# Kernel tuning notes

Hardware: AMD Instinct MI355X
Metric: run time of the kernel (lower is better)

## Reference

```python
import jax, jax.numpy as jnp
import numpy as np

N_HEAD = 16

def setup_inputs() -> dict:
    key = jax.random.key(0)
    k1, k2, k3, k4, k5 = jax.random.split(key, 5)
    B, T, C = 4, 2048, 1024
    s = 0.02
    x = jax.random.normal(k1, (B, T, C), dtype=jnp.float32)
    W_attn = jax.random.normal(k2, (C, 3 * C), dtype=jnp.float32) * s
    b_attn = jnp.zeros((3 * C,), dtype=jnp.float32)
    W_proj = jax.random.normal(k3, (C, C), dtype=jnp.float32) * s
    b_proj = jnp.zeros((C,), dtype=jnp.float32)
    return {"x": x, "W_attn": W_attn, "b_attn": b_attn, "W_proj": W_proj, "b_proj": b_proj}

def reference(x, W_attn, b_attn, W_proj, b_proj):
    B, T, C = x.shape
    H = N_HEAD
    hd = C // H
    qkv = x @ W_attn + b_attn                       # [B,T,3C]
    q, k, v = jnp.split(qkv, 3, axis=-1)            # each [B,T,C]
    # [B,H,T,hd]
    q = q.reshape(B, T, H, hd).transpose(0, 2, 1, 3)
    k = k.reshape(B, T, H, hd).transpose(0, 2, 1, 3)
    v = v.reshape(B, T, H, hd).transpose(0, 2, 1, 3)
    att = jnp.einsum('bhqd,bhkd->bhqk', q, k) * (1.0 / jnp.sqrt(jnp.float32(hd)))
    causal = jnp.tril(jnp.ones((T, T), dtype=bool))
    att = jnp.where(causal[None, None], att, jnp.float32(-jnp.inf))
    att = jax.nn.softmax(att, axis=-1)
    y = jnp.einsum('bhqk,bhkd->bhqd', att, v)       # [B,H,T,hd]
    y = y.transpose(0, 2, 1, 3).reshape(B, T, C)
    return y @ W_proj + b_proj
```

## Files before the change

### kernel.cpp

```cpp
#include <hip/hip_runtime.h>
#include <hip/hip_bf16.h>

typedef __bf16 bf16x8 __attribute__((ext_vector_type(8)));
typedef float f32x4 __attribute__((ext_vector_type(4)));

static __device__ __forceinline__ unsigned short f32_to_bf16(float f) {
    union { float f; unsigned u; } v; v.f = f;
    unsigned u = v.u;
    u += 0x7FFFu + ((u >> 16) & 1u);
    return (unsigned short)(u >> 16);
}

static __device__ __forceinline__ void async_load16(const unsigned short* g,
                                                    unsigned short* l) {
    __builtin_amdgcn_global_load_lds(
        (__attribute__((address_space(1))) const unsigned int*)(const void*)g,
        (__attribute__((address_space(3))) unsigned int*)(void*)l,
        16, 0, 0);
}

__global__ void cast_f32_bf16(const float* __restrict__ src,
                              unsigned short* __restrict__ dst, int n4) {
    int i = blockIdx.x * blockDim.x + threadIdx.x;
    if (i < n4) {
        float4 f = ((const float4*)src)[i];
        ushort4 o;
        o.x = f32_to_bf16(f.x); o.y = f32_to_bf16(f.y);
        o.z = f32_to_bf16(f.z); o.w = f32_to_bf16(f.w);
        ((ushort4*)dst)[i] = o;
    }
}

__global__ void transpose_cast(const float* __restrict__ src,
                               unsigned short* __restrict__ dst, int R, int C) {
    __shared__ float tile[32][33];
    int c0 = blockIdx.x * 32, r0 = blockIdx.y * 32;
    int tx = threadIdx.x, ty = threadIdx.y;
    #pragma unroll
    for (int i = 0; i < 32; i += 8)
        tile[ty + i][tx] = src[(long)(r0 + ty + i) * C + c0 + tx];
    __syncthreads();
    #pragma unroll
    for (int i = 0; i < 32; i += 8)
        dst[(long)(c0 + ty + i) * R + r0 + tx] = f32_to_bf16(tile[tx][ty + i]);
}

template<bool OUT_BF16>
__global__ __launch_bounds__(256) void gemm_bt_bias(
    const unsigned short* __restrict__ A,
    const unsigned short* __restrict__ Bt,
    const float* __restrict__ bias,
    void* __restrict__ Cout,
    int M, int N, int K)
{
    __shared__ __align__(16) unsigned short As[128 * 32];
    __shared__ __align__(16) unsigned short Bs[128 * 32];

    const int tid  = threadIdx.x;
    const int m0   = blockIdx.x * 128;
    const int n0   = blockIdx.y * 128;
    const int w    = tid >> 6, lane = tid & 63;
    const int quad = lane >> 4, lr = lane & 15;
    const int wm   = (w >> 1) * 64, wn = (w & 1) * 64;

    f32x4 acc[4][4];
    #pragma unroll
    for (int i = 0; i < 4; i++)
        #pragma unroll
        for (int j = 0; j < 4; j++)
            acc[i][j] = (f32x4){0.f, 0.f, 0.f, 0.f};

    const int srow = lane >> 2;
    const int soff = (lane & 3) * 8;
    const unsigned short* gA0 = &A [(long)(m0 + w * 16 + srow) * K + soff];
    const unsigned short* gA1 = &A [(long)(m0 + 64 + w * 16 + srow) * K + soff];
    const unsigned short* gB0 = &Bt[(long)(n0 + w * 16 + srow) * K + soff];
    const unsigned short* gB1 = &Bt[(long)(n0 + 64 + w * 16 + srow) * K + soff];
    unsigned short* lA0 = &As[(w * 16) * 32];
    unsigned short* lA1 = &As[(64 + w * 16) * 32];
    unsigned short* lB0 = &Bs[(w * 16) * 32];
    unsigned short* lB1 = &Bs[(64 + w * 16) * 32];

    for (int k0 = 0; k0 < K; k0 += 32) {
        __syncthreads();
        async_load16(gA0 + k0, lA0);
        async_load16(gA1 + k0, lA1);
        async_load16(gB0 + k0, lB0);
        async_load16(gB1 + k0, lB1);
        __syncthreads();

        bf16x8 af[4], bfr[4];
        #pragma unroll
        for (int i = 0; i < 4; i++)
            af[i] = *(const bf16x8*)&As[(wm + i * 16 + lr) * 32 + quad * 8];
        #pragma unroll
        for (int j = 0; j < 4; j++)
            bfr[j] = *(const bf16x8*)&Bs[(wn + j * 16 + lr) * 32 + quad * 8];
        #pragma unroll
        for (int i = 0; i < 4; i++)
            #pragma unroll
            for (int j = 0; j < 4; j++)
                acc[i][j] = __builtin_amdgcn_mfma_f32_16x16x32_bf16(af[i], bfr[j], acc[i][j], 0, 0, 0);
    }

    #pragma unroll
    for (int i = 0; i < 4; i++) {
        #pragma unroll
        for (int j = 0; j < 4; j++) {
            int gcol = n0 + wn + j * 16 + lr;
            float bv = bias[gcol];
            #pragma unroll
            for (int r = 0; r < 4; r++) {
                int grow = m0 + wm + i * 16 + quad * 4 + r;
                float v = acc[i][j][r] + bv;
                if (OUT_BF16)
                    ((unsigned short*)Cout)[(long)grow * N + gcol] = f32_to_bf16(v);
                else
                    ((float*)Cout)[(long)grow * N + gcol] = v;
            }
        }
    }
}

__global__ __launch_bounds__(256) void transpose_v(
    const unsigned short* __restrict__ qkv,
    unsigned short* __restrict__ vT,
    int T, int C3, int C, int H)
{
    __shared__ __align__(16) unsigned short tile[64 * 72];
    const int tid = threadIdx.x;
    const int t0 = blockIdx.x * 64, h = blockIdx.y, b = blockIdx.z;
    const long ibase = ((long)b * T + t0) * C3 + 2 * C + h * 64;
    #pragma unroll
    for (int c = tid; c < 512; c += 256) {
        int r = c >> 3, off = (c & 7) * 8;
        *(uint4*)&tile[r * 72 + off] = *(const uint4*)&qkv[ibase + (long)r * C3 + off];
    }
    __syncthreads();
    const long obase = (long)((b * H + h) * 64) * T + t0;
    #pragma unroll
    for (int c = tid; c < 512; c += 256) {
        int d = c & 63, tc = c >> 6;
        unsigned short tmp[8];
        #pragma unroll
        for (int j = 0; j < 8; j++)
            tmp[j] = tile[(tc * 8 + j) * 72 + d];
        *(uint4*)&vT[obase + (long)d * T + tc * 8] = *(const uint4*)tmp;
    }
}

__global__ __launch_bounds__(256, 2) void attn_mfma(
    const unsigned short* __restrict__ qkv,
    const unsigned short* __restrict__ vT,
    unsigned short* __restrict__ yb,
    int T, int C3, int C, int H, int NT)
{
    constexpr int SQ = 72;
    __shared__ __align__(16) unsigned short Qs[128 * SQ];
    __shared__ __align__(16) unsigned short Ks[64 * SQ];
    __shared__ __align__(16) unsigned short Vs[64 * SQ];
    __shared__ __align__(16) unsigned short Ps[128 * SQ];

    const int tid = threadIdx.x;
    const int h   = blockIdx.y;
    const int b   = blockIdx.z;
    const long rowbase = (long)b * T;
    const long vtbase  = (long)((b * H + h) * 64) * T;

    const int w = tid >> 6, lane = tid & 63;
    const int quad = lane >> 4, lr = lane & 15;

    const int r0 = tid >> 3, off0 = (tid & 7) * 8;
    const int r1 = r0 + 32;

    const float scale2 = 0.1803368801111244f;

    for (int t = 0; t < 2; t++) {
        const int qt = (t == 0) ? blockIdx.x : (NT - 1 - blockIdx.x);
        const int q0 = qt * 128;
        const int nb = 2 * qt + 2;

        __syncthreads();

        #pragma unroll
        for (int i = 0; i < 4; i++)
            *(uint4*)&Qs[(r0 + i * 32) * SQ + off0] =
                *(const uint4*)&qkv[(rowbase + q0 + r0 + i * 32) * C3 + h * 64 + off0];

        uint4 pk0, pk1, pv0, pv1;
        {
            long g0 = (rowbase + r0) * (long)C3 + C + h * 64 + off0;
            long g1 = (rowbase + r1) * (long)C3 + C + h * 64 + off0;
            pk0 = *(const uint4*)&qkv[g0];
            pk1 = *(const uint4*)&qkv[g1];
            pv0 = *(const uint4*)&vT[vtbase + (long)r0 * T + off0];
            pv1 = *(const uint4*)&vT[vtbase + (long)r1 * T + off0];
        }

        f32x4 oA[2][4];
        float lp[8];
        #pragma unroll
        for (int st = 0; st < 2; st++)
            #pragma unroll
            for (int j = 0; j < 4; j++) oA[st][j] = (f32x4){0.f, 0.f, 0.f, 0.f};
        #pragma unroll
        for (int i = 0; i < 8; i++) lp[i] = 0.f;

        const int wrow0 = w * 32;
        const int wrowmax = q0 + wrow0 + 31;

        for (int kb = 0; kb < nb; kb++) {
            __syncthreads();
            *(uint4*)&Ks[r0 * SQ + off0] = pk0;
            *(uint4*)&Ks[r1 * SQ + off0] = pk1;
            *(uint4*)&Vs[r0 * SQ + off0] = pv0;
            *(uint4*)&Vs[r1 * SQ + off0] = pv1;
            __syncthreads();

            if (kb + 1 < nb) {
                long g0 = (rowbase + (kb + 1) * 64 + r0) * (long)C3 + C + h * 64 + off0;
                long g1 = (rowbase + (kb + 1) * 64 + r1) * (long)C3 + C + h * 64 + off0;
                pk0 = *(const uint4*)&qkv[g0];
                pk1 = *(const uint4*)&qkv[g1];
                pv0 = *(const uint4*)&vT[vtbase + (long)r0 * T + (kb + 1) * 64 + off0];
                pv1 = *(const uint4*)&vT[vtbase + (long)r1 * T + (kb + 1) * 64 + off0];
            }

            if (kb * 64 > wrowmax) continue;

            f32x4 sA[2][4];
            #pragma unroll
            for (int st = 0; st < 2; st++)
                #pragma unroll
                for (int j = 0; j < 4; j++) sA[st][j] = (f32x4){0.f, 0.f, 0.f, 0.f};
            #pragma unroll
            for (int ks = 0; ks < 2; ks++) {
                bf16x8 aq0 = *(const bf16x8*)&Qs[(wrow0 + lr) * SQ + ks * 32 + quad * 8];
                bf16x8 aq1 = *(const bf16x8*)&Qs[(wrow0 + 16 + lr) * SQ + ks * 32 + quad * 8];
                #pragma unroll
                for (int jt = 0; jt < 4; jt++) {
                    bf16x8 bk = *(const bf16x8*)&Ks[(jt * 16 + lr) * SQ + ks * 32 + quad * 8];
                    sA[0][jt] = __builtin_amdgcn_mfma_f32_16x16x32_bf16(aq0, bk, sA[0][jt], 0, 0, 0);
                    sA[1][jt] = __builtin_amdgcn_mfma_f32_16x16x32_bf16(aq1, bk, sA[1][jt], 0, 0, 0);
                }
            }

            const bool diag = (kb >= nb - 2);
            #pragma unroll
            for (int st = 0; st < 2; st++) {
                #pragma unroll
                for (int r = 0; r < 4; r++) {
                    int rowin = q0 + wrow0 + st * 16 + quad * 4 + r;
                    #pragma unroll
                    for (int jt = 0; jt < 4; jt++) {
                        float sv = sA[st][jt][r] * scale2;
                        if (diag && (kb * 64 + jt * 16 + lr) > rowin) sv = -1e30f;
                        float p = exp2f(fminf(sv, 80.f));
                        lp[st * 4 + r] += p;
                        Ps[(wrow0 + st * 16 + quad * 4 + r) * SQ + jt * 16 + lr] = f32_to_bf16(p);
                    }
                }
            }

            #pragma unroll
            for (int ks = 0; ks < 2; ks++) {
                bf16x8 ap0 = *(const bf16x8*)&Ps[(wrow0 + lr) * SQ + ks * 32 + quad * 8];
                bf16x8 ap1 = *(const bf16x8*)&Ps[(wrow0 + 16 + lr) * SQ + ks * 32 + quad * 8];
                #pragma unroll
                for (int jt = 0; jt < 4; jt++) {
                    bf16x8 bv = *(const bf16x8*)&Vs[(jt * 16 + lr) * SQ + ks * 32 + quad * 8];
                    oA[0][jt] = __builtin_amdgcn_mfma_f32_16x16x32_bf16(ap0, bv, oA[0][jt], 0, 0, 0);
                    oA[1][jt] = __builtin_amdgcn_mfma_f32_16x16x32_bf16(ap1, bv, oA[1][jt], 0, 0, 0);
                }
            }
        }

        #pragma unroll
        for (int st = 0; st < 2; st++) {
            #pragma unroll
            for (int r = 0; r < 4; r++) {
                float l = lp[st * 4 + r];
                l += __shfl_xor(l, 1);
                l += __shfl_xor(l, 2);
                l += __shfl_xor(l, 4);
                l += __shfl_xor(l, 8);
                float inv = 1.f / l;
                long grow = rowbase + q0 + wrow0 + st * 16 + quad * 4 + r;
                #pragma unroll
                for (int jt = 0; jt < 4; jt++)
                    yb[grow * C + h * 64 + jt * 16 + lr] = f32_to_bf16(oA[st][jt][r] * inv);
            }
        }
    }
}

extern "C" void kernel_launch(void* const* d_in, const int* in_sizes, int n_in,
                              void* d_out, int out_size, void* d_ws, size_t ws_size,
                              hipStream_t stream) {
    const float* x      = (const float*)d_in[0];
    const float* W_attn = (const float*)d_in[1];
    const float* b_attn = (const float*)d_in[2];
    const float* W_proj = (const float*)d_in[3];
    const float* b_proj = (const float*)d_in[4];
    float* out = (float*)d_out;

    const int B = 4, T = 2048, C = 1024, H = 16;
    const int M  = B * T;
    const int C3 = 3 * C;
    const int NT = T / 128;

    char* ws = (char*)d_ws;
    size_t off = 0;
    auto carve = [&](size_t bytes) {
        char* p = ws + off;
        off += (bytes + 255) & ~(size_t)255;
        return p;
    };
    unsigned short* xb   = (unsigned short*)carve((size_t)M * C * 2);
    unsigned short* wat  = (unsigned short*)carve((size_t)C3 * C * 2);
    unsigned short* wpt  = (unsigned short*)carve((size_t)C * C * 2);
    unsigned short* qkvb = (unsigned short*)carve((size_t)M * C3 * 2);
    unsigned short* ybuf = (unsigned short*)carve((size_t)M * C * 2);
    unsigned short* vTb  = xb;

    cast_f32_bf16<<<(M * C / 4 + 255) / 256, 256, 0, stream>>>(x, xb, M * C / 4);
    transpose_cast<<<dim3(C3 / 32, C / 32), dim3(32, 8), 0, stream>>>(W_attn, wat, C, C3);
    transpose_cast<<<dim3(C / 32, C / 32), dim3(32, 8), 0, stream>>>(W_proj, wpt, C, C);

    gemm_bt_bias<true><<<dim3(M / 128, C3 / 128), 256, 0, stream>>>(
        xb, wat, b_attn, qkvb, M, C3, C);

    transpose_v<<<dim3(T / 64, H, B), 256, 0, stream>>>(qkvb, vTb, T, C3, C, H);

    attn_mfma<<<dim3(NT / 2, H, B), 256, 0, stream>>>(qkvb, vTb, ybuf, T, C3, C, H, NT);

    gemm_bt_bias<false><<<dim3(M / 128, C / 128), 256, 0, stream>>>(
        ybuf, wpt, b_proj, out, M, C, C);
}
```

Baseline: 297.4 us.

## Fold softmax scale into QKV GEMM and keep Q fragments in registers

```diff
diff --git a/kernel.cpp b/kernel.cpp
--- a/kernel.cpp
+++ b/kernel.cpp
@@ -51,7 +51,7 @@
     const unsigned short* __restrict__ Bt,
     const float* __restrict__ bias,
     void* __restrict__ Cout,
-    int M, int N, int K)
+    int M, int N, int K, int scale_ncols, float scale)
 {
     __shared__ __align__(16) unsigned short As[128 * 32];
     __shared__ __align__(16) unsigned short Bs[128 * 32];
@@ -109,10 +109,11 @@
         for (int j = 0; j < 4; j++) {
             int gcol = n0 + wn + j * 16 + lr;
             float bv = bias[gcol];
+            float sc = (gcol < scale_ncols) ? scale : 1.0f;
             #pragma unroll
             for (int r = 0; r < 4; r++) {
                 int grow = m0 + wm + i * 16 + quad * 4 + r;
-                float v = acc[i][j][r] + bv;
+                float v = (acc[i][j][r] + bv) * sc;
                 if (OUT_BF16)
                     ((unsigned short*)Cout)[(long)grow * N + gcol] = f32_to_bf16(v);
                 else
@@ -149,14 +150,13 @@
     }
 }
 
-__global__ __launch_bounds__(256, 2) void attn_mfma(
+__global__ __launch_bounds__(256, 4) void attn_mfma(
     const unsigned short* __restrict__ qkv,
     const unsigned short* __restrict__ vT,
     unsigned short* __restrict__ yb,
     int T, int C3, int C, int H, int NT)
 {
     constexpr int SQ = 72;
-    __shared__ __align__(16) unsigned short Qs[128 * SQ];
     __shared__ __align__(16) unsigned short Ks[64 * SQ];
     __shared__ __align__(16) unsigned short Vs[64 * SQ];
     __shared__ __align__(16) unsigned short Ps[128 * SQ];
@@ -173,19 +173,21 @@
     const int r0 = tid >> 3, off0 = (tid & 7) * 8;
     const int r1 = r0 + 32;
 
-    const float scale2 = 0.1803368801111244f;
-
     for (int t = 0; t < 2; t++) {
         const int qt = (t == 0) ? blockIdx.x : (NT - 1 - blockIdx.x);
         const int q0 = qt * 128;
         const int nb = 2 * qt + 2;
 
-        __syncthreads();
-
-        #pragma unroll
-        for (int i = 0; i < 4; i++)
-            *(uint4*)&Qs[(r0 + i * 32) * SQ + off0] =
-                *(const uint4*)&qkv[(rowbase + q0 + r0 + i * 32) * C3 + h * 64 + off0];
+        const int wrow0 = w * 32;
+        const int wrowmax = q0 + wrow0 + 31;
+
+        bf16x8 aq[2][2];
+        #pragma unroll
+        for (int st = 0; st < 2; st++)
+            #pragma unroll
+            for (int ks = 0; ks < 2; ks++)
+                aq[st][ks] = *(const bf16x8*)&qkv[
+                    (rowbase + q0 + wrow0 + st * 16 + lr) * (long)C3 + h * 64 + ks * 32 + quad * 8];
 
         uint4 pk0, pk1, pv0, pv1;
         {
@@ -206,9 +208,6 @@
         #pragma unroll
         for (int i = 0; i < 8; i++) lp[i] = 0.f;
 
-        const int wrow0 = w * 32;
-        const int wrowmax = q0 + wrow0 + 31;
-
         for (int kb = 0; kb < nb; kb++) {
             __syncthreads();
             *(uint4*)&Ks[r0 * SQ + off0] = pk0;
@@ -235,13 +234,11 @@
                 for (int j = 0; j < 4; j++) sA[st][j] = (f32x4){0.f, 0.f, 0.f, 0.f};
             #pragma unroll
             for (int ks = 0; ks < 2; ks++) {
-                bf16x8 aq0 = *(const bf16x8*)&Qs[(wrow0 + lr) * SQ + ks * 32 + quad * 8];
-                bf16x8 aq1 = *(const bf16x8*)&Qs[(wrow0 + 16 + lr) * SQ + ks * 32 + quad * 8];
                 #pragma unroll
                 for (int jt = 0; jt < 4; jt++) {
                     bf16x8 bk = *(const bf16x8*)&Ks[(jt * 16 + lr) * SQ + ks * 32 + quad * 8];
-                    sA[0][jt] = __builtin_amdgcn_mfma_f32_16x16x32_bf16(aq0, bk, sA[0][jt], 0, 0, 0);
-                    sA[1][jt] = __builtin_amdgcn_mfma_f32_16x16x32_bf16(aq1, bk, sA[1][jt], 0, 0, 0);
+                    sA[0][jt] = __builtin_amdgcn_mfma_f32_16x16x32_bf16(aq[0][ks], bk, sA[0][jt], 0, 0, 0);
+                    sA[1][jt] = __builtin_amdgcn_mfma_f32_16x16x32_bf16(aq[1][ks], bk, sA[1][jt], 0, 0, 0);
                 }
             }
 
@@ -253,9 +250,9 @@
                     int rowin = q0 + wrow0 + st * 16 + quad * 4 + r;
                     #pragma unroll
                     for (int jt = 0; jt < 4; jt++) {
-                        float sv = sA[st][jt][r] * scale2;
+                        float sv = sA[st][jt][r];
                         if (diag && (kb * 64 + jt * 16 + lr) > rowin) sv = -1e30f;
-                        float p = exp2f(fminf(sv, 80.f));
+                        float p = exp2f(sv);
                         lp[st * 4 + r] += p;
                         Ps[(wrow0 + st * 16 + quad * 4 + r) * SQ + jt * 16 + lr] = f32_to_bf16(p);
                     }
@@ -308,6 +305,7 @@
     const int M  = B * T;
     const int C3 = 3 * C;
     const int NT = T / 128;
+    const float scale2 = 0.18033688011112042f;
 
     char* ws = (char*)d_ws;
     size_t off = 0;
@@ -328,12 +326,12 @@
     transpose_cast<<<dim3(C / 32, C / 32), dim3(32, 8), 0, stream>>>(W_proj, wpt, C, C);
 
     gemm_bt_bias<true><<<dim3(M / 128, C3 / 128), 256, 0, stream>>>(
-        xb, wat, b_attn, qkvb, M, C3, C);
+        xb, wat, b_attn, qkvb, M, C3, C, C, scale2);
 
     transpose_v<<<dim3(T / 64, H, B), 256, 0, stream>>>(qkvb, vTb, T, C3, C, H);
 
     attn_mfma<<<dim3(NT / 2, H, B), 256, 0, stream>>>(qkvb, vTb, ybuf, T, C3, C, H, NT);
 
     gemm_bt_bias<false><<<dim3(M / 128, C / 128), 256, 0, stream>>>(
-        ybuf, wpt, b_proj, out, M, C, C);
-}
+        ybuf, wpt, b_proj, out, M, C, C, 0, 1.0f);
+}
```

Result: slower. 336.4 us (+13.1%).
